# Kernel tuning notes

Measured on AMD Instinct MI355X. Metric: run time of the kernel, lower is better.

Reference implementation:

```python
import jax, jax.numpy as jnp
import numpy as np

N = 100000
E = 600000
G = 8
HID = 128
HEADS = 4
C = HID // HEADS  # 32


def setup_inputs() -> dict:
    key = jax.random.key(0)
    ks = jax.random.split(key, 32)
    s = 0.05
    node_numeric = jax.random.normal(ks[0], (N, 8), jnp.float32)
    node_cat0 = jax.random.randint(ks[1], (N,), 0, 32)
    node_cat1 = jax.random.randint(ks[2], (N,), 0, 64)
    edge_numeric = jax.random.normal(ks[3], (E, 4), jnp.float32)
    edge_cat0 = jax.random.randint(ks[4], (E,), 0, 16)
    edge_cat1 = jax.random.randint(ks[5], (E,), 0, 100)
    src = jax.random.randint(ks[6], (E,), 0, N)
    dst = jax.random.randint(ks[7], (E,), 0, N)
    dst = jnp.where(dst == src, (dst + 1) % N, dst)  # GATConv removes self-loops before adding its own
    edge_index = jnp.stack([src, dst])
    batch = jnp.sort(jax.random.randint(ks[8], (N,), 0, G))
    recipe = jax.random.normal(ks[9], (G, 16), jnp.float32)
    return dict(
        node_numeric=node_numeric, node_cat0=node_cat0, node_cat1=node_cat1,
        edge_numeric=edge_numeric, edge_cat0=edge_cat0, edge_cat1=edge_cat1,
        edge_index=edge_index, batch=batch, recipe=recipe,
        emb_node0=jax.random.normal(ks[10], (32, 6), jnp.float32) * s,
        emb_node1=jax.random.normal(ks[11], (64, 8), jnp.float32) * s,
        emb_edge0=jax.random.normal(ks[12], (16, 4), jnp.float32) * s,
        emb_edge1=jax.random.normal(ks[13], (100, 10), jnp.float32) * s,
        W_in=jax.random.normal(ks[14], (38, HID), jnp.float32) * s,
        b_in=jnp.zeros((HID,), jnp.float32),
        W_edge=jax.random.normal(ks[15], (18, HID), jnp.float32) * s,
        b_edge=jnp.zeros((HID,), jnp.float32),
        gat_lin=jax.random.normal(ks[16], (3, HID, HID), jnp.float32) * s,
        gat_lin_edge=jax.random.normal(ks[17], (3, HID, HID), jnp.float32) * s,
        att_src=jax.random.normal(ks[18], (3, HEADS, C), jnp.float32) * s,
        att_dst=jax.random.normal(ks[19], (3, HEADS, C), jnp.float32) * s,
        att_edge=jax.random.normal(ks[20], (3, HEADS, C), jnp.float32) * s,
        gat_bias=jnp.zeros((3, HID), jnp.float32),
        W_r1=jax.random.normal(ks[21], (HID, HID), jnp.float32) * s,
        b_r1=jnp.zeros((HID,), jnp.float32),
        W_r2=jax.random.normal(ks[22], (HID, 1), jnp.float32) * s,
        b_r2=jnp.zeros((1,), jnp.float32),
    )


def _segment_softmax(logits, seg, num):
    m = jax.ops.segment_max(logits, seg, num_segments=num)
    ex = jnp.exp(logits - m[seg])
    s = jax.ops.segment_sum(ex, seg, num_segments=num)
    return ex / s[seg]


def _forward(node_numeric, edge_numeric, recipe,
             emb_node0, emb_node1, emb_edge0, emb_edge1,
             W_in, b_in, W_edge, b_edge,
             gat_lin, gat_lin_edge, att_src, att_dst, att_edge, gat_bias,
             W_r1, b_r1, W_r2, b_r2,
             node_cat0, node_cat1, edge_cat0, edge_cat1, edge_index, batch):
    n = node_numeric.shape[0]
    src, dst = edge_index[0], edge_index[1]
    # node encoding: numeric + categorical embeddings + broadcast recipe
    h = jnp.concatenate([node_numeric, emb_node0[node_cat0], emb_node1[node_cat1], recipe[batch]], axis=1)
    h = jax.nn.relu(h @ W_in + b_in)
    # edge encoding (shared across GAT layers)
    e = jnp.concatenate([edge_numeric, emb_edge0[edge_cat0], emb_edge1[edge_cat1]], axis=1)
    e = e @ W_edge + b_edge
    # self-loops with fill_value='mean': per-dst mean of incoming edge_attr
    cnt = jax.ops.segment_sum(jnp.ones((e.shape[0],), e.dtype), dst, num_segments=n)
    loop = jax.ops.segment_sum(e, dst, num_segments=n) / jnp.maximum(cnt, 1.0)[:, None]
    ar = jnp.arange(n)
    src_a = jnp.concatenate([src, ar])
    dst_a = jnp.concatenate([dst, ar])
    e_a = jnp.concatenate([e, loop], axis=0)  # [E+N, HID]
    for l in range(gat_lin.shape[0]):
        x = (h @ gat_lin[l]).reshape(n, HEADS, C)          # shared lin_src/lin_dst
        ee = (e_a @ gat_lin_edge[l]).reshape(-1, HEADS, C)
        a_s = jnp.sum(x * att_src[l], axis=-1)   # [N, HEADS]
        a_d = jnp.sum(x * att_dst[l], axis=-1)
        a_e = jnp.sum(ee * att_edge[l], axis=-1)  # [E+N, HEADS]
        logits = jax.nn.leaky_relu(a_s[src_a] + a_d[dst_a] + a_e, negative_slope=0.2)
        alpha = _segment_softmax(logits, dst_a, n)  # segment softmax over dst
        out = jax.ops.segment_sum(x[src_a] * alpha[:, :, None], dst_a, num_segments=n)
        h = jax.nn.relu(out.reshape(n, HID) + gat_bias[l])  # dropout off (eval)
    g = jax.ops.segment_sum(h, batch, num_segments=G)  # global_add_pool
    g = jax.nn.relu(g @ W_r1 + b_r1)
    return g @ W_r2 + b_r2  # [G, 1]


def reference(node_numeric, node_cat0, node_cat1, edge_numeric, edge_cat0, edge_cat1,
              edge_index, batch, recipe,
              emb_node0, emb_node1, emb_edge0, emb_edge1,
              W_in, b_in, W_edge, b_edge,
              gat_lin, gat_lin_edge, att_src, att_dst, att_edge, gat_bias,
              W_r1, b_r1, W_r2, b_r2):
    return _forward(node_numeric, edge_numeric, recipe,
                    emb_node0, emb_node1, emb_edge0, emb_edge1,
                    W_in, b_in, W_edge, b_edge,
                    gat_lin, gat_lin_edge, att_src, att_dst, att_edge, gat_bias,
                    W_r1, b_r1, W_r2, b_r2,
                    node_cat0, node_cat1, edge_cat0, edge_cat1, edge_index, batch)
```

## Files before the change

### kernel.cpp

```cpp
#include <hip/hip_runtime.h>
#include <math.h>

#define HID 128

typedef float f32x4 __attribute__((ext_vector_type(4)));
typedef short bf16x8 __attribute__((ext_vector_type(8)));
typedef unsigned int uint32;

__device__ __forceinline__ float leaky02(float z) { return z >= 0.f ? z : 0.2f * z; }
__device__ __forceinline__ unsigned short f2bf(float f) {
  uint32 u = __float_as_uint(f);
  u = (u + 0x7fff + ((u >> 16) & 1)) >> 16;
  return (unsigned short)u;
}
__device__ __forceinline__ float bf2f(uint32 us) { return __uint_as_float(us << 16); }

__global__ void k_enc(const float* __restrict__ nodenum, const int* __restrict__ c0,
                      const int* __restrict__ c1, const int* __restrict__ batch,
                      const float* __restrict__ recipe,
                      const float* __restrict__ e0, const float* __restrict__ e1,
                      const float* __restrict__ Win, const float* __restrict__ bin,
                      unsigned short* __restrict__ hb, int n) {
  __shared__ float f[8][40];
  __shared__ int idx[8][3];
  int t = threadIdx.x;
  int col = t & 127;
  int half = t >> 7;
  float w[40];
#pragma unroll
  for (int k = 0; k < 38; k++) w[k] = Win[k * 128 + col];
  w[38] = 0.f;
  w[39] = 0.f;
  float bias = bin[col];
  int ntiles = (n + 7) / 8;
  for (int tile = blockIdx.x; tile < ntiles; tile += gridDim.x) {
    int base = tile * 8;
    if (t < 64) {
      int r = t >> 3, k = t & 7;
      int v = base + r;
      f[r][k] = (v < n) ? nodenum[(size_t)v * 8 + k] : 0.f;
    } else if (t < 88) {
      int j = t - 64;
      int r = j / 3, which = j - r * 3;
      int v = base + r;
      int val = 0;
      if (v < n) val = (which == 0) ? c0[v] : ((which == 1) ? c1[v] : batch[v]);
      idx[r][which] = val;
    } else if (t >= 240) {
      int r = t - 240;
      if (r < 8) { f[r][38] = 0.f; f[r][39] = 0.f; }
    }
    __syncthreads();
    if (t < 240) {
      int r = t / 30, k = t - r * 30;
      float val;
      if (k < 6) val = e0[idx[r][0] * 6 + k];
      else if (k < 14) val = e1[idx[r][1] * 8 + (k - 6)];
      else val = recipe[idx[r][2] * 16 + (k - 14)];
      f[r][8 + k] = val;
    }
    __syncthreads();
#pragma unroll
    for (int rr = 0; rr < 4; rr++) {
      int r = half * 4 + rr;
      int v = base + r;
      float acc = bias;
#pragma unroll
      for (int k4 = 0; k4 < 10; k4++) {
        float4 fv = *(const float4*)(&f[r][k4 * 4]);
        acc += fv.x * w[k4 * 4] + fv.y * w[k4 * 4 + 1] + fv.z * w[k4 * 4 + 2] +
               fv.w * w[k4 * 4 + 3];
      }
      if (v < n) hb[(size_t)v * 128 + col] = f2bf(fmaxf(acc, 0.f));
    }
    __syncthreads();
  }
}

__global__ void k_prep(const float* __restrict__ gle, const float* __restrict__ atte,
                       const float* __restrict__ We, const float* __restrict__ be,
                       float* __restrict__ P, float* __restrict__ q) {
  __shared__ float M[128 * 4];
  int t = threadIdx.x;
  for (int l = 0; l < 3; l++) {
    {
      int k = t;
#pragma unroll
      for (int hh = 0; hh < 4; hh++) {
        float acc = 0.f;
        for (int c = 0; c < 32; c++)
          acc += gle[l * 16384 + k * 128 + hh * 32 + c] * atte[l * 128 + hh * 32 + c];
        M[k * 4 + hh] = acc;
      }
    }
    __syncthreads();
    if (t < 72) {
      int j = t >> 2, hh = t & 3;
      float acc = 0.f;
      for (int k = 0; k < 128; k++) acc += We[j * 128 + k] * M[k * 4 + hh];
      P[(l * 18 + j) * 4 + hh] = acc;
    }
    if (t < 4) {
      float acc = 0.f;
      for (int k = 0; k < 128; k++) acc += be[k] * M[k * 4 + t];
      q[l * 4 + t] = acc;
    }
    __syncthreads();
  }
}

__global__ void k_ae(const float* __restrict__ enum_, const int* __restrict__ ec0,
                     const int* __restrict__ ec1, const int* __restrict__ dst,
                     const float* __restrict__ ee0, const float* __restrict__ ee1,
                     const float* __restrict__ P, const float* __restrict__ q,
                     float* __restrict__ ae, int* __restrict__ cnt, int E) {
  __shared__ float Ps[216];
  __shared__ float qs[12];
  int t = threadIdx.x;
  for (int i = t; i < 216; i += 256) Ps[i] = P[i];
  if (t < 12) qs[t] = q[t];
  __syncthreads();
  int i = blockIdx.x * 256 + t;
  if (i >= E) return;
  float raw[18];
  float4 nm = *(const float4*)(enum_ + (size_t)i * 4);
  raw[0] = nm.x; raw[1] = nm.y; raw[2] = nm.z; raw[3] = nm.w;
  int a0 = ec0[i], a1 = ec1[i];
  float4 eb0 = *(const float4*)(ee0 + a0 * 4);
  raw[4] = eb0.x; raw[5] = eb0.y; raw[6] = eb0.z; raw[7] = eb0.w;
#pragma unroll
  for (int j = 0; j < 10; j++) raw[8 + j] = ee1[a1 * 10 + j];
  atomicAdd(&cnt[dst[i]], 1);
#pragma unroll
  for (int l = 0; l < 3; l++) {
    float o[4];
#pragma unroll
    for (int hh = 0; hh < 4; hh++) {
      float acc = qs[l * 4 + hh];
#pragma unroll
      for (int j = 0; j < 18; j++) acc += raw[j] * Ps[(l * 18 + j) * 4 + hh];
      o[hh] = acc;
    }
    *(float4*)(ae + (size_t)i * 12 + l * 4) = make_float4(o[0], o[1], o[2], o[3]);
  }
}

__global__ void k_reorder(const float* __restrict__ ae, const int* __restrict__ csr,
                          const int* __restrict__ srcarr, float* __restrict__ ae3,
                          int* __restrict__ srcc, int E) {
  int j = blockIdx.x * 256 + threadIdx.x;
  if (j >= E) return;
  int eid = csr[j];
  srcc[j] = srcarr[eid];
  const float4* p = (const float4*)(ae + (size_t)eid * 12);
  float4 a = p[0], b = p[1], c = p[2];
  *(float4*)(ae3 + ((size_t)0 * E + j) * 4) = a;
  *(float4*)(ae3 + ((size_t)1 * E + j) * 4) = b;
  *(float4*)(ae3 + ((size_t)2 * E + j) * 4) = c;
}

__global__ void k_loopmean(const float* __restrict__ ae3, const int* __restrict__ rowptr,
                           float* __restrict__ aeL, int n, int E) {
  int v = blockIdx.x * 256 + threadIdx.x;
  if (v >= n) return;
  int beg = rowptr[v], end = rowptr[v + 1];
  float inv = (end > beg) ? 1.f / (float)(end - beg) : 0.f;
#pragma unroll
  for (int l = 0; l < 3; l++) {
    float4 s = make_float4(0.f, 0.f, 0.f, 0.f);
    const float4* base = (const float4*)(ae3 + (size_t)l * E * 4);
    for (int j = beg; j < end; j++) {
      float4 a = base[j];
      s.x += a.x; s.y += a.y; s.z += a.z; s.w += a.w;
    }
    *(float4*)(aeL + ((size_t)l * n + v) * 4) =
        make_float4(s.x * inv, s.y * inv, s.z * inv, s.w * inv);
  }
}

__global__ void k_scan1(const int* __restrict__ cnt, int* __restrict__ excl,
                        int* __restrict__ bsum, int n) {
  __shared__ int sh[256];
  int t = threadIdx.x;
  int i = blockIdx.x * 256 + t;
  int v = (i < n) ? cnt[i] : 0;
  sh[t] = v;
  __syncthreads();
  for (int off = 1; off < 256; off <<= 1) {
    int add = (t >= off) ? sh[t - off] : 0;
    __syncthreads();
    sh[t] += add;
    __syncthreads();
  }
  if (i < n) excl[i] = sh[t] - v;
  if (t == 255) bsum[blockIdx.x] = sh[255];
}

__global__ void k_scan2(int* __restrict__ bsum, int nb) {
  __shared__ int sh[512];
  int t = threadIdx.x;
  int v = (t < nb) ? bsum[t] : 0;
  sh[t] = v;
  __syncthreads();
  for (int off = 1; off < 512; off <<= 1) {
    int add = (t >= off) ? sh[t - off] : 0;
    __syncthreads();
    sh[t] += add;
    __syncthreads();
  }
  if (t < nb) bsum[t] = sh[t] - v;
}

__global__ void k_scan3(int* __restrict__ rowptr, const int* __restrict__ boff,
                        int* __restrict__ cursor, int n, int E) {
  int i = blockIdx.x * 256 + threadIdx.x;
  if (i < n) {
    int val = rowptr[i] + boff[i >> 8];
    rowptr[i] = val;
    cursor[i] = val;
  }
  if (i == 0) rowptr[n] = E;
}

__global__ void k_fill(const int* __restrict__ dst, int* __restrict__ cursor,
                       int* __restrict__ csr, int E) {
  int i = blockIdx.x * 256 + threadIdx.x;
  if (i >= E) return;
  int pos = atomicAdd(&cursor[dst[i]], 1);
  csr[pos] = i;
}

__global__ void k_x(const unsigned short* __restrict__ hb, const float* __restrict__ W,
                    const float* __restrict__ att_s, const float* __restrict__ att_d,
                    unsigned short* __restrict__ xb, float* __restrict__ a_s,
                    float* __restrict__ a_d, int n) {
  __shared__ unsigned short hs[64 * 128];
  int t = threadIdx.x;
  int w = t >> 6, l = t & 63;
  int ch = w >> 2, wr = w & 3;
  int lr = l & 15, lg = l >> 4;
  bf16x8 bfrag[4][4];
#pragma unroll
  for (int ct = 0; ct < 4; ct++) {
#pragma unroll
    for (int ks = 0; ks < 4; ks++) {
      int col = ch * 64 + ct * 16 + lr;
      int k0 = ks * 32 + lg * 8;
      bf16x8 fr;
#pragma unroll
      for (int j = 0; j < 8; j++) fr[j] = (short)f2bf(W[(k0 + j) * 128 + col]);
      bfrag[ct][ks] = fr;
    }
  }
  float avs[4], avd[4];
#pragma unroll
  for (int ct = 0; ct < 4; ct++) {
    avs[ct] = att_s[ch * 64 + ct * 16 + lr];
    avd[ct] = att_d[ch * 64 + ct * 16 + lr];
  }
  for (int tb = blockIdx.x * 64; tb < n; tb += gridDim.x * 64) {
    __syncthreads();
#pragma unroll
    for (int i = 0; i < 2; i++) {
      int idx = t + i * 512;
      int r = idx >> 4, c = idx & 15;
      uint4 vv = make_uint4(0, 0, 0, 0);
      if (tb + r < n) vv = *(const uint4*)(hb + (size_t)(tb + r) * 128 + c * 8);
      *(uint4*)(&hs[r * 128 + ((c ^ (r & 7)) * 8)]) = vv;
    }
    __syncthreads();
    f32x4 acc[4];
#pragma unroll
    for (int ct = 0; ct < 4; ct++) acc[ct] = (f32x4){0.f, 0.f, 0.f, 0.f};
#pragma unroll
    for (int ks = 0; ks < 4; ks++) {
      int r = wr * 16 + lr;
      int c = ks * 4 + lg;
      bf16x8 a = *(const bf16x8*)(&hs[r * 128 + ((c ^ (r & 7)) * 8)]);
#pragma unroll
      for (int ct = 0; ct < 4; ct++)
        acc[ct] = __builtin_amdgcn_mfma_f32_16x16x32_bf16(a, bfrag[ct][ks], acc[ct], 0, 0, 0);
    }
#pragma unroll
    for (int j = 0; j < 4; j++) {
      int row = tb + wr * 16 + lg * 4 + j;
      bool ok = row < n;
      if (ok) {
#pragma unroll
        for (int ct = 0; ct < 4; ct++)
          xb[(size_t)row * 128 + ch * 64 + ct * 16 + lr] = f2bf(acc[ct][j]);
      }
      float psA = acc[0][j] * avs[0] + acc[1][j] * avs[1];
      float pdA = acc[0][j] * avd[0] + acc[1][j] * avd[1];
      float psB = acc[2][j] * avs[2] + acc[3][j] * avs[3];
      float pdB = acc[2][j] * avd[2] + acc[3][j] * avd[3];
#pragma unroll
      for (int m = 1; m <= 8; m <<= 1) {
        psA += __shfl_xor(psA, m); pdA += __shfl_xor(pdA, m);
        psB += __shfl_xor(psB, m); pdB += __shfl_xor(pdB, m);
      }
      if (lr == 0 && ok) {
        a_s[(size_t)row * 4 + ch * 2] = psA;
        a_s[(size_t)row * 4 + ch * 2 + 1] = psB;
        a_d[(size_t)row * 4 + ch * 2] = pdA;
        a_d[(size_t)row * 4 + ch * 2 + 1] = pdB;
      }
    }
  }
}

__global__ void k_agg(const unsigned short* __restrict__ xb, const float* __restrict__ a_s,
                      const float* __restrict__ a_d, const float* __restrict__ ae3,
                      const float* __restrict__ aeL,
                      const int* __restrict__ rowptr, const int* __restrict__ srcc,
                      const float* __restrict__ bias,
                      unsigned short* __restrict__ hbout, int n, int E, int l) {
  int wid = threadIdx.x >> 6;
  int v = blockIdx.x * 4 + wid;
  if (v >= n) return;
  int lane = threadIdx.x & 63;
  int el = lane >> 2;
  int hh = lane & 3;
  float ad_own = a_d[(size_t)v * 4 + hh];
  float as_own = a_s[(size_t)v * 4 + hh];
  float aeL_own = aeL[((size_t)l * n + v) * 4 + hh];
  float m_own = leaky02(as_own + ad_own + aeL_own);
  float s_own = 1.f;
  int c2 = lane * 2;
  int headO = lane >> 4;
  uint32 wv = *(const uint32*)(xb + (size_t)v * 128 + c2);
  float a0 = bf2f(wv & 0xffff);
  float a1 = bf2f(wv >> 16);
  int beg = rowptr[v], end = rowptr[v + 1];
  const float* aeB = ae3 + (size_t)l * E * 4;
  for (int cb = beg; cb < end; cb += 16) {
    int ne = end - cb;
    if (ne > 16) ne = 16;
    float logit = -1e30f;
    int srcE = 0;
    if (el < ne) {
      int j = cb + el;
      srcE = srcc[j];
      float asrc = a_s[(size_t)srcE * 4 + hh];
      float aev = aeB[(size_t)j * 4 + hh];
      logit = leaky02(asrc + ad_own + aev);
    }
    float cm = logit;
    cm = fmaxf(cm, __shfl_xor(cm, 4));
    cm = fmaxf(cm, __shfl_xor(cm, 8));
    cm = fmaxf(cm, __shfl_xor(cm, 16));
    cm = fmaxf(cm, __shfl_xor(cm, 32));
    float mn_own = fmaxf(m_own, cm);
    float p = (el < ne) ? __expf(logit - mn_own) : 0.f;
    float ps = p;
    ps += __shfl_xor(ps, 4);
    ps += __shfl_xor(ps, 8);
    ps += __shfl_xor(ps, 16);
    ps += __shfl_xor(ps, 32);
    float c_own = __expf(m_own - mn_own);
    m_own = mn_own;
    s_own = s_own * c_own + ps;
    float cO = __shfl(c_own, headO);
    a0 *= cO;
    a1 *= cO;
    int e = 0;
    for (; e + 2 <= ne; e += 2) {
      int se0 = __builtin_amdgcn_readlane(srcE, e * 4);
      int se1 = __builtin_amdgcn_readlane(srcE, e * 4 + 4);
      float p0 = __shfl(p, e * 4 + headO);
      float p1 = __shfl(p, e * 4 + 4 + headO);
      uint32 x0 = *(const uint32*)(xb + (size_t)se0 * 128 + c2);
      uint32 x1 = *(const uint32*)(xb + (size_t)se1 * 128 + c2);
      a0 += p0 * bf2f(x0 & 0xffff) + p1 * bf2f(x1 & 0xffff);
      a1 += p0 * bf2f(x0 >> 16) + p1 * bf2f(x1 >> 16);
    }
    if (e < ne) {
      int se = __builtin_amdgcn_readlane(srcE, e * 4);
      float pC = __shfl(p, e * 4 + headO);
      uint32 xw = *(const uint32*)(xb + (size_t)se * 128 + c2);
      a0 += pC * bf2f(xw & 0xffff);
      a1 += pC * bf2f(xw >> 16);
    }
  }
  float sO = __shfl(s_own, headO);
  float r0 = fmaxf(a0 / sO + bias[l * HID + c2], 0.f);
  float r1 = fmaxf(a1 / sO + bias[l * HID + c2 + 1], 0.f);
  uint32 pk = (uint32)f2bf(r0) | ((uint32)f2bf(r1) << 16);
  *(uint32*)(hbout + (size_t)v * HID + c2) = pk;
}

__global__ void k_pool(const unsigned short* __restrict__ hb, const int* __restrict__ batch,
                       float* __restrict__ g, int n) {
  int t = threadIdx.x;
  int per = (n + gridDim.x - 1) / gridDim.x;
  int start = blockIdx.x * per;
  int end = min(n, start + per);
  float acc = 0.f;
  int cur = -1;
  for (int v = start; v < end; v++) {
    int b = batch[v];
    if (b != cur) {
      if (cur >= 0) atomicAdd(&g[cur * 128 + t], acc);
      acc = 0.f;
      cur = b;
    }
    acc += bf2f((uint32)hb[(size_t)v * 128 + t]);
  }
  if (cur >= 0) atomicAdd(&g[cur * 128 + t], acc);
}

__global__ void k_head(const float* __restrict__ g, const float* __restrict__ Wr1,
                       const float* __restrict__ br1, const float* __restrict__ Wr2,
                       const float* __restrict__ br2, float* __restrict__ out, int G_) {
  __shared__ float gl[8 * 128];
  __shared__ float red[128];
  int t = threadIdx.x;
  for (int i = t; i < G_ * 128; i += 128) gl[i] = g[i];
  __syncthreads();
  for (int i = 0; i < G_; i++) {
    float acc = br1[t];
    for (int k = 0; k < 128; k++) acc += gl[i * 128 + k] * Wr1[k * 128 + t];
    float hv = fmaxf(acc, 0.f);
    red[t] = hv * Wr2[t];
    __syncthreads();
    if (t == 0) {
      float s = br2[0];
      for (int k = 0; k < 128; k++) s += red[k];
      out[i] = s;
    }
    __syncthreads();
  }
}

extern "C" void kernel_launch(void* const* d_in, const int* in_sizes, int n_in,
                              void* d_out, int out_size, void* d_ws, size_t ws_size,
                              hipStream_t stream) {
  const float* node_numeric = (const float*)d_in[0];
  const int* node_cat0 = (const int*)d_in[1];
  const int* node_cat1 = (const int*)d_in[2];
  const float* edge_numeric = (const float*)d_in[3];
  const int* edge_cat0 = (const int*)d_in[4];
  const int* edge_cat1 = (const int*)d_in[5];
  const int* edge_index = (const int*)d_in[6];
  const int* batch = (const int*)d_in[7];
  const float* recipe = (const float*)d_in[8];
  const float* emb_node0 = (const float*)d_in[9];
  const float* emb_node1 = (const float*)d_in[10];
  const float* emb_edge0 = (const float*)d_in[11];
  const float* emb_edge1 = (const float*)d_in[12];
  const float* W_in = (const float*)d_in[13];
  const float* b_in = (const float*)d_in[14];
  const float* W_edge = (const float*)d_in[15];
  const float* b_edge = (const float*)d_in[16];
  const float* gat_lin = (const float*)d_in[17];
  const float* gat_lin_edge = (const float*)d_in[18];
  const float* att_src = (const float*)d_in[19];
  const float* att_dst = (const float*)d_in[20];
  const float* att_edge = (const float*)d_in[21];
  const float* gat_bias = (const float*)d_in[22];
  const float* W_r1 = (const float*)d_in[23];
  const float* b_r1 = (const float*)d_in[24];
  const float* W_r2 = (const float*)d_in[25];
  const float* b_r2 = (const float*)d_in[26];

  int N = in_sizes[0] / 8;
  int E = in_sizes[3] / 4;
  int Gn = in_sizes[8] / 16;
  const int* srcArr = edge_index;
  const int* dstArr = edge_index + E;

  char* ws = (char*)d_ws;
  size_t o = 0;
  auto alloc = [&](size_t b) {
    char* p = ws + o;
    o = (o + b + 255) & ~(size_t)255;
    return p;
  };
  unsigned short* hbf = (unsigned short*)alloc((size_t)N * 128 * 2);
  unsigned short* xbf = (unsigned short*)alloc((size_t)N * 128 * 2);
  float* ae = (float*)alloc((size_t)E * 12 * 4);
  float* ae3 = (float*)alloc((size_t)E * 12 * 4);
  float* aeL = (float*)alloc((size_t)N * 12 * 4);
  float* a_s = (float*)alloc((size_t)N * 4 * 4);
  float* a_d = (float*)alloc((size_t)N * 4 * 4);
  float* P = (float*)alloc(216 * 4);
  float* q = (float*)alloc(12 * 4);
  int* cnt = (int*)alloc((size_t)N * 4);
  int* rowptr = (int*)alloc((size_t)(N + 1) * 4);
  int* cursor = (int*)alloc((size_t)N * 4);
  int* bsum = (int*)alloc(512 * 4);
  int* csr = (int*)alloc((size_t)E * 4);
  int* srcc = (int*)alloc((size_t)E * 4);
  float* g = (float*)alloc((size_t)Gn * 128 * 4);
  (void)ws_size;

  (void)hipMemsetAsync(cnt, 0, (size_t)N * 4, stream);
  (void)hipMemsetAsync(g, 0, (size_t)Gn * 128 * 4, stream);

  int nbl = (N + 255) / 256;
  int ebl = (E + 255) / 256;

  k_enc<<<2048, 256, 0, stream>>>(node_numeric, node_cat0, node_cat1, batch, recipe,
                                  emb_node0, emb_node1, W_in, b_in, hbf, N);
  k_prep<<<1, 128, 0, stream>>>(gat_lin_edge, att_edge, W_edge, b_edge, P, q);
  k_ae<<<ebl, 256, 0, stream>>>(edge_numeric, edge_cat0, edge_cat1, dstArr,
                                emb_edge0, emb_edge1, P, q, ae, cnt, E);
  k_scan1<<<nbl, 256, 0, stream>>>(cnt, rowptr, bsum, N);
  k_scan2<<<1, 512, 0, stream>>>(bsum, nbl);
  k_scan3<<<nbl, 256, 0, stream>>>(rowptr, bsum, cursor, N, E);
  k_fill<<<ebl, 256, 0, stream>>>(dstArr, cursor, csr, E);
  k_reorder<<<ebl, 256, 0, stream>>>(ae, csr, srcArr, ae3, srcc, E);
  k_loopmean<<<nbl, 256, 0, stream>>>(ae3, rowptr, aeL, N, E);

  for (int l = 0; l < 3; l++) {
    k_x<<<512, 512, 0, stream>>>(hbf, gat_lin + l * 16384, att_src + l * 128,
                                 att_dst + l * 128, xbf, a_s, a_d, N);
    k_agg<<<(N + 3) / 4, 256, 0, stream>>>(xbf, a_s, a_d, ae3, aeL, rowptr, srcc,
                                           gat_bias, hbf, N, E, l);
  }
  k_pool<<<1024, 128, 0, stream>>>(hbf, batch, g, N);
  k_head<<<1, 128, 0, stream>>>(g, W_r1, b_r1, W_r2, b_r2, (float*)d_out, Gn);
}
```

Measured before the change: 445.4 us.

## Fuse CSR fill and edge reorder into edge-attention kernel; simplify agg addressing

Degree counting is split into a small kernel, and the edge-attention kernel now runs after the scan, claiming CSR slots with atomics. It writes the edge logits and source ids directly in CSR order. This removes the fill and reorder kernels and the intermediate ae and csr buffers, cutting a full pass of scattered reads and writes over edge data. It also adds launch bounds to the projection kernel and uses 32-bit byte-offset addressing with cheaper bf16 unpacking in the aggregation kernel. The 32-bit offsets assume the node feature buffer stays under 4 GB.

```diff
diff --git a/kernel.cpp b/kernel.cpp
--- a/kernel.cpp
+++ b/kernel.cpp
@@ -14,6 +14,8 @@
   return (unsigned short)u;
 }
 __device__ __forceinline__ float bf2f(uint32 us) { return __uint_as_float(us << 16); }
+__device__ __forceinline__ float bflo(uint32 w) { return __uint_as_float(w << 16); }
+__device__ __forceinline__ float bfhi(uint32 w) { return __uint_as_float(w & 0xffff0000u); }
 
 __global__ void k_enc(const float* __restrict__ nodenum, const int* __restrict__ c0,
                       const int* __restrict__ c1, const int* __restrict__ batch,
@@ -109,11 +111,18 @@
   }
 }
 
+__global__ void k_deg(const int* __restrict__ dst, int* __restrict__ cnt, int E) {
+  int i = blockIdx.x * 256 + threadIdx.x;
+  if (i < E) atomicAdd(&cnt[dst[i]], 1);
+}
+
 __global__ void k_ae(const float* __restrict__ enum_, const int* __restrict__ ec0,
                      const int* __restrict__ ec1, const int* __restrict__ dst,
+                     const int* __restrict__ srcarr,
                      const float* __restrict__ ee0, const float* __restrict__ ee1,
                      const float* __restrict__ P, const float* __restrict__ q,
-                     float* __restrict__ ae, int* __restrict__ cnt, int E) {
+                     int* __restrict__ cursor, float* __restrict__ ae3,
+                     int* __restrict__ srcc, int E) {
   __shared__ float Ps[216];
   __shared__ float qs[12];
   int t = threadIdx.x;
@@ -130,7 +139,9 @@
   raw[4] = eb0.x; raw[5] = eb0.y; raw[6] = eb0.z; raw[7] = eb0.w;
 #pragma unroll
   for (int j = 0; j < 10; j++) raw[8 + j] = ee1[a1 * 10 + j];
-  atomicAdd(&cnt[dst[i]], 1);
+  int d = dst[i];
+  int pos = atomicAdd(&cursor[d], 1);
+  srcc[pos] = srcarr[i];
 #pragma unroll
   for (int l = 0; l < 3; l++) {
     float o[4];
@@ -141,22 +152,8 @@
       for (int j = 0; j < 18; j++) acc += raw[j] * Ps[(l * 18 + j) * 4 + hh];
       o[hh] = acc;
     }
-    *(float4*)(ae + (size_t)i * 12 + l * 4) = make_float4(o[0], o[1], o[2], o[3]);
-  }
-}
-
-__global__ void k_reorder(const float* __restrict__ ae, const int* __restrict__ csr,
-                          const int* __restrict__ srcarr, float* __restrict__ ae3,
-                          int* __restrict__ srcc, int E) {
-  int j = blockIdx.x * 256 + threadIdx.x;
-  if (j >= E) return;
-  int eid = csr[j];
-  srcc[j] = srcarr[eid];
-  const float4* p = (const float4*)(ae + (size_t)eid * 12);
-  float4 a = p[0], b = p[1], c = p[2];
-  *(float4*)(ae3 + ((size_t)0 * E + j) * 4) = a;
-  *(float4*)(ae3 + ((size_t)1 * E + j) * 4) = b;
-  *(float4*)(ae3 + ((size_t)2 * E + j) * 4) = c;
+    *(float4*)(ae3 + ((size_t)l * E + pos) * 4) = make_float4(o[0], o[1], o[2], o[3]);
+  }
 }
 
 __global__ void k_loopmean(const float* __restrict__ ae3, const int* __restrict__ rowptr,
@@ -222,18 +219,11 @@
   if (i == 0) rowptr[n] = E;
 }
 
-__global__ void k_fill(const int* __restrict__ dst, int* __restrict__ cursor,
-                       int* __restrict__ csr, int E) {
-  int i = blockIdx.x * 256 + threadIdx.x;
-  if (i >= E) return;
-  int pos = atomicAdd(&cursor[dst[i]], 1);
-  csr[pos] = i;
-}
-
-__global__ void k_x(const unsigned short* __restrict__ hb, const float* __restrict__ W,
-                    const float* __restrict__ att_s, const float* __restrict__ att_d,
-                    unsigned short* __restrict__ xb, float* __restrict__ a_s,
-                    float* __restrict__ a_d, int n) {
+__global__ void __launch_bounds__(512, 4)
+k_x(const unsigned short* __restrict__ hb, const float* __restrict__ W,
+    const float* __restrict__ att_s, const float* __restrict__ att_d,
+    unsigned short* __restrict__ xb, float* __restrict__ a_s,
+    float* __restrict__ a_d, int n) {
   __shared__ unsigned short hs[64 * 128];
   int t = threadIdx.x;
   int w = t >> 6, l = t & 63;
@@ -328,9 +318,11 @@
   float s_own = 1.f;
   int c2 = lane * 2;
   int headO = lane >> 4;
-  uint32 wv = *(const uint32*)(xb + (size_t)v * 128 + c2);
-  float a0 = bf2f(wv & 0xffff);
-  float a1 = bf2f(wv >> 16);
+  const char* xB = (const char*)xb;
+  uint32 coff = (uint32)c2 * 2u;
+  uint32 wv = *(const uint32*)(xB + ((uint32)v << 8) + coff);
+  float a0 = bflo(wv);
+  float a1 = bfhi(wv);
   int beg = rowptr[v], end = rowptr[v + 1];
   const float* aeB = ae3 + (size_t)l * E * 4;
   for (int cb = beg; cb < end; cb += 16) {
@@ -369,17 +361,17 @@
       int se1 = __builtin_amdgcn_readlane(srcE, e * 4 + 4);
       float p0 = __shfl(p, e * 4 + headO);
       float p1 = __shfl(p, e * 4 + 4 + headO);
-      uint32 x0 = *(const uint32*)(xb + (size_t)se0 * 128 + c2);
-      uint32 x1 = *(const uint32*)(xb + (size_t)se1 * 128 + c2);
-      a0 += p0 * bf2f(x0 & 0xffff) + p1 * bf2f(x1 & 0xffff);
-      a1 += p0 * bf2f(x0 >> 16) + p1 * bf2f(x1 >> 16);
+      uint32 x0 = *(const uint32*)(xB + ((uint32)se0 << 8) + coff);
+      uint32 x1 = *(const uint32*)(xB + ((uint32)se1 << 8) + coff);
+      a0 += p0 * bflo(x0) + p1 * bflo(x1);
+      a1 += p0 * bfhi(x0) + p1 * bfhi(x1);
     }
     if (e < ne) {
       int se = __builtin_amdgcn_readlane(srcE, e * 4);
       float pC = __shfl(p, e * 4 + headO);
-      uint32 xw = *(const uint32*)(xb + (size_t)se * 128 + c2);
-      a0 += pC * bf2f(xw & 0xffff);
-      a1 += pC * bf2f(xw >> 16);
+      uint32 xw = *(const uint32*)(xB + ((uint32)se << 8) + coff);
+      a0 += pC * bflo(xw);
+      a1 += pC * bfhi(xw);
     }
   }
   float sO = __shfl(s_own, headO);
@@ -478,7 +470,6 @@
   };
   unsigned short* hbf = (unsigned short*)alloc((size_t)N * 128 * 2);
   unsigned short* xbf = (unsigned short*)alloc((size_t)N * 128 * 2);
-  float* ae = (float*)alloc((size_t)E * 12 * 4);
   float* ae3 = (float*)alloc((size_t)E * 12 * 4);
   float* aeL = (float*)alloc((size_t)N * 12 * 4);
   float* a_s = (float*)alloc((size_t)N * 4 * 4);
@@ -489,7 +480,6 @@
   int* rowptr = (int*)alloc((size_t)(N + 1) * 4);
   int* cursor = (int*)alloc((size_t)N * 4);
   int* bsum = (int*)alloc(512 * 4);
-  int* csr = (int*)alloc((size_t)E * 4);
   int* srcc = (int*)alloc((size_t)E * 4);
   float* g = (float*)alloc((size_t)Gn * 128 * 4);
   (void)ws_size;
@@ -503,13 +493,12 @@
   k_enc<<<2048, 256, 0, stream>>>(node_numeric, node_cat0, node_cat1, batch, recipe,
                                   emb_node0, emb_node1, W_in, b_in, hbf, N);
   k_prep<<<1, 128, 0, stream>>>(gat_lin_edge, att_edge, W_edge, b_edge, P, q);
-  k_ae<<<ebl, 256, 0, stream>>>(edge_numeric, edge_cat0, edge_cat1, dstArr,
-                                emb_edge0, emb_edge1, P, q, ae, cnt, E);
+  k_deg<<<ebl, 256, 0, stream>>>(dstArr, cnt, E);
   k_scan1<<<nbl, 256, 0, stream>>>(cnt, rowptr, bsum, N);
   k_scan2<<<1, 512, 0, stream>>>(bsum, nbl);
   k_scan3<<<nbl, 256, 0, stream>>>(rowptr, bsum, cursor, N, E);
-  k_fill<<<ebl, 256, 0, stream>>>(dstArr, cursor, csr, E);
-  k_reorder<<<ebl, 256, 0, stream>>>(ae, csr, srcArr, ae3, srcc, E);
+  k_ae<<<ebl, 256, 0, stream>>>(edge_numeric, edge_cat0, edge_cat1, dstArr, srcArr,
+                                emb_edge0, emb_edge1, P, q, cursor, ae3, srcc, E);
   k_loopmean<<<nbl, 256, 0, stream>>>(ae3, rowptr, aeL, N, E);
 
   for (int l = 0; l < 3; l++) {
```

New measurement: 435.4 us. 1.02x faster.
